# Kernel tuning notes

Measured on AMD Instinct MI355X. Metric: run time of the kernel, lower is better.

## Reference

```python
import jax, jax.numpy as jnp
import numpy as np

BATCH, TIMESTEPS, DIM, OUT = 64, 512, 1024, 1024


def setup_inputs() -> dict:
    key = jax.random.key(0)
    k1, k2, k3, k4, k5, k6 = jax.random.split(key, 6)
    # glorot-normal-ish scales for params
    def glorot(k, shape):
        fan_in, fan_out = shape[0], shape[-1]
        std = (2.0 / (fan_in + fan_out)) ** 0.5
        return jax.random.normal(k, shape, dtype=jnp.float32) * std
    return {
        "inputs": jax.random.normal(k1, (BATCH, TIMESTEPS, DIM), dtype=jnp.float32),
        "prev_state": jax.random.normal(k2, (BATCH, OUT), dtype=jnp.float32),
        "Wa": glorot(k3, (OUT, OUT)),
        "Ua": glorot(k4, (DIM, OUT)),
        "Va": glorot(k5, (OUT, 1)),
        "Ba": glorot(k6, (1, OUT)),
    }


def reference(inputs, prev_state, Wa, Ua, Va, Ba):
    # WaS: [B, 1, OUT] broadcast over timesteps
    WaS = jnp.einsum("bo,op->bp", prev_state, Wa)[:, None, :]
    # UaH: [B, T, OUT]
    UaH = jnp.einsum("btd,do->bto", inputs, Ua)
    scores = jnp.tanh(UaH + WaS + Ba)            # [B, T, OUT]
    scores = jax.nn.relu(scores @ Va)            # [B, T, 1]
    sm = jax.nn.softmax(scores, axis=1)          # softmax over timesteps
    context_vector = jnp.sum(inputs * sm, axis=1)  # [B, DIM]
    return context_vector
```

## Files before the change

### kernel.cpp

```cpp
#include <hip/hip_runtime.h>


#define NBATCH 64
#define NT     512
#define NDIM   1024
#define NOUT   1024

typedef _Float16 h8 __attribute__((ext_vector_type(8)));
typedef _Float16 h4 __attribute__((ext_vector_type(4)));
typedef float f16v __attribute__((ext_vector_type(16)));

__device__ __forceinline__ float tanh_fast(float x) {
    float e = __expf(2.0f * x);
    return 1.0f - 2.0f * __builtin_amdgcn_rcpf(e + 1.0f);
}

__global__ __launch_bounds__(256) void k_pack_ua(const float* __restrict__ Ua,
                                                 _Float16* __restrict__ B16) {
    int t = blockIdx.x * 256 + threadIdx.x;
    int nn = t & 31, kg = (t >> 5) & 1, ks = (t >> 6) & 63, nt = t >> 12;
    int n = (nt << 5) + nn;
    int kbase = (ks << 4) + (kg << 3);
    h8 v;
#pragma unroll
    for (int j = 0; j < 8; ++j) v[j] = (_Float16)Ua[(size_t)(kbase + j) * 1024 + n];
    *(h8*)(B16 + ((size_t)t << 3)) = v;
}

__global__ __launch_bounds__(256) void k_was_part(const float* __restrict__ ps,
                                                  const float* __restrict__ Wa,
                                                  float* __restrict__ part) {
    int oc = blockIdx.x, b = blockIdx.y, tid = threadIdx.x;
    const float4* Wa4 = (const float4*)Wa;
    const float* psb = ps + b * 1024;
    float4 acc = {0.f, 0.f, 0.f, 0.f};
    int o0 = oc * 128;
#pragma unroll 4
    for (int o = o0; o < o0 + 128; ++o) {
        float s = psb[o];
        float4 wv = Wa4[o * 256 + tid];
        acc.x += s * wv.x; acc.y += s * wv.y; acc.z += s * wv.z; acc.w += s * wv.w;
    }
    ((float4*)part)[((oc << 6) + b) * 256 + tid] = acc;
}

__global__ __launch_bounds__(256) void k_was_reduce(const float* __restrict__ part,
                                                    const float* __restrict__ Ba,
                                                    float* __restrict__ wsWaS) {
    int b = blockIdx.x, tid = threadIdx.x;
    const float4* p4 = (const float4*)part;
    float4 acc = ((const float4*)Ba)[tid];
#pragma unroll
    for (int oc = 0; oc < 8; ++oc) {
        float4 v = p4[((oc << 6) + b) * 256 + tid];
        acc.x += v.x; acc.y += v.y; acc.z += v.z; acc.w += v.w;
    }
    ((float4*)wsWaS)[b * 256 + tid] = acc;
}

#define ASH_STRIDE 136
__global__ __launch_bounds__(256, 2) void k_fused_gemm(
    const float* __restrict__ inputs, const _Float16* __restrict__ B16,
    const float* __restrict__ wsWaS, const float* __restrict__ Va,
    float* __restrict__ scores)
{
    __shared__ _Float16 Ash[2][64 * ASH_STRIDE];
    __shared__ float scoreSh[64];
    const int tid = threadIdx.x;
    const int lane = tid & 63, wv = tid >> 6;
    const int l31 = lane & 31, lhi = lane >> 5;
    const int r0 = blockIdx.x * 64;
    const int b = r0 >> 9;
    const int srow = tid >> 2, sq = tid & 3;
    const float4* srcBase = (const float4*)inputs + (size_t)(r0 + srow) * 256 + sq * 8;

    if (tid < 64) scoreSh[tid] = 0.0f;

    float4 vA[8];
#pragma unroll
    for (int j = 0; j < 8; ++j) vA[j] = srcBase[j];
    {
        _Float16* dst = &Ash[0][srow * ASH_STRIDE + sq * 32];
#pragma unroll
        for (int j = 0; j < 8; ++j) {
            float4 v = vA[j];
            *(h4*)(dst + j * 4) =
                (h4){ (_Float16)v.x, (_Float16)v.y, (_Float16)v.z, (_Float16)v.w };
        }
    }
    __syncthreads();

    for (int pass = 0; pass < 2; ++pass) {
        const int c0w = pass * 512 + wv * 128;
        const int ntb = c0w >> 5;
        f16v acc[2][4];
#pragma unroll
        for (int rt = 0; rt < 2; ++rt)
#pragma unroll
            for (int ct = 0; ct < 4; ++ct)
#pragma unroll
                for (int e = 0; e < 16; ++e) acc[rt][ct][e] = 0.0f;

        for (int kc = 0; kc < 8; ++kc) {
            const int buf = kc & 1;
            const bool pf = !(pass == 1 && kc == 7);
            if (pf) {
                const float4* src = srcBase + (((kc + 1) & 7) << 5);
#pragma unroll
                for (int j = 0; j < 8; ++j) vA[j] = src[j];
            }
#pragma unroll
            for (int ks8 = 0; ks8 < 8; ++ks8) {
                const int ks = kc * 8 + ks8;
                h8 a0 = *(const h8*)&Ash[buf][l31 * ASH_STRIDE + ks8 * 16 + lhi * 8];
                h8 a1 = *(const h8*)&Ash[buf][(32 + l31) * ASH_STRIDE + ks8 * 16 + lhi * 8];
                h8 bf[4];
#pragma unroll
                for (int ct = 0; ct < 4; ++ct)
                    bf[ct] = *(const h8*)(B16 +
                        ((size_t)(((ntb + ct) << 6) + ks) << 9) + lane * 8);
#pragma unroll
                for (int ct = 0; ct < 4; ++ct) {
                    acc[0][ct] = __builtin_amdgcn_mfma_f32_32x32x16_f16(a0, bf[ct], acc[0][ct], 0, 0, 0);
                    acc[1][ct] = __builtin_amdgcn_mfma_f32_32x32x16_f16(a1, bf[ct], acc[1][ct], 0, 0, 0);
                }
            }
            if (pf) {
                _Float16* dst = &Ash[buf ^ 1][srow * ASH_STRIDE + sq * 32];
#pragma unroll
                for (int j = 0; j < 8; ++j) {
                    float4 v = vA[j];
                    *(h4*)(dst + j * 4) =
                        (h4){ (_Float16)v.x, (_Float16)v.y, (_Float16)v.z, (_Float16)v.w };
                }
            }
            __syncthreads();
        }
        float wsv[4], vav[4];
#pragma unroll
        for (int ct = 0; ct < 4; ++ct) {
            int n = c0w + ct * 32 + l31;
            wsv[ct] = wsWaS[b * 1024 + n];
            vav[ct] = Va[n];
        }
#pragma unroll
        for (int rt = 0; rt < 2; ++rt) {
#pragma unroll
            for (int i = 0; i < 16; ++i) {
                float s = 0.0f;
#pragma unroll
                for (int ct = 0; ct < 4; ++ct)
                    s += tanh_fast(acc[rt][ct][i] + wsv[ct]) * vav[ct];
                s += __shfl_xor(s, 1);
                s += __shfl_xor(s, 2);
                s += __shfl_xor(s, 4);
                s += __shfl_xor(s, 8);
                s += __shfl_xor(s, 16);
                if (l31 == 0) {
                    int row = rt * 32 + (i & 3) + ((i >> 2) << 3) + (lhi << 2);
                    atomicAdd(&scoreSh[row], s);
                }
            }
        }
    }
    __syncthreads();
    if (tid < 64) scores[r0 + tid] = fmaxf(scoreSh[tid], 0.0f);
}

__global__ __launch_bounds__(256) void k_softmax(const float* __restrict__ scores,
                                                 float* __restrict__ sm) {
    int b = blockIdx.x, tid = threadIdx.x;
    __shared__ float red[256];
    const float* sb = scores + b * 512;
    float s0 = sb[tid], s1 = sb[tid + 256];
    red[tid] = fmaxf(s0, s1);
    __syncthreads();
    for (int st = 128; st > 0; st >>= 1) {
        if (tid < st) red[tid] = fmaxf(red[tid], red[tid + st]);
        __syncthreads();
    }
    float m = red[0];
    __syncthreads();
    float e0 = __expf(s0 - m), e1 = __expf(s1 - m);
    red[tid] = e0 + e1;
    __syncthreads();
    for (int st = 128; st > 0; st >>= 1) {
        if (tid < st) red[tid] += red[tid + st];
        __syncthreads();
    }
    float inv = 1.0f / red[0];
    sm[b * 512 + tid] = e0 * inv;
    sm[b * 512 + 256 + tid] = e1 * inv;
}

__global__ __launch_bounds__(256) void k_ctx_part(const float* __restrict__ inputs,
                                                  const float* __restrict__ sm,
                                                  float* __restrict__ part) {
    int ts = blockIdx.x, b = blockIdx.y, tid = threadIdx.x;
    const float4* inF4 = (const float4*)inputs;
    float4 acc = {0.f, 0.f, 0.f, 0.f};
    int t0 = ts * 64;
#pragma unroll 8
    for (int t = t0; t < t0 + 64; ++t) {
        float wgt = sm[b * 512 + t];
        float4 x = inF4[(size_t)(b * 512 + t) * 256 + tid];
        acc.x += wgt * x.x; acc.y += wgt * x.y; acc.z += wgt * x.z; acc.w += wgt * x.w;
    }
    ((float4*)part)[((ts << 6) + b) * 256 + tid] = acc;
}

__global__ __launch_bounds__(256) void k_ctx_reduce(const float* __restrict__ part,
                                                    float* __restrict__ out) {
    int g = blockIdx.x * 256 + threadIdx.x;
    const float4* p4 = (const float4*)part;
    float4 acc = p4[g];
#pragma unroll
    for (int s = 1; s < 8; ++s) {
        float4 v = p4[s * 16384 + g];
        acc.x += v.x; acc.y += v.y; acc.z += v.z; acc.w += v.w;
    }
    ((float4*)out)[g] = acc;
}

extern "C" void kernel_launch(void* const* d_in, const int* in_sizes, int n_in,
                              void* d_out, int out_size, void* d_ws, size_t ws_size,
                              hipStream_t stream) {
    const float* inputs = (const float*)d_in[0];
    const float* prev   = (const float*)d_in[1];
    const float* Wa     = (const float*)d_in[2];
    const float* Ua     = (const float*)d_in[3];
    const float* Va     = (const float*)d_in[4];
    const float* Ba     = (const float*)d_in[5];
    float* out = (float*)d_out;

    char* ws = (char*)d_ws;
    _Float16* B16   = (_Float16*)(ws);
    float* wasPart  = (float*)(ws + (2u << 20));
    float* wsWaS    = (float*)(ws + (4u << 20));
    float* scores   = (float*)(ws + (4u << 20) + (256u << 10));
    float* sm       = (float*)(ws + (4u << 20) + (384u << 10));
    float* ctxPart  = (float*)(ws + (4u << 20) + (512u << 10));

    hipLaunchKernelGGL(k_pack_ua,    dim3(512),    dim3(256), 0, stream, Ua, B16);
    hipLaunchKernelGGL(k_was_part,   dim3(8, 64),  dim3(256), 0, stream, prev, Wa, wasPart);
    hipLaunchKernelGGL(k_was_reduce, dim3(64),     dim3(256), 0, stream, wasPart, Ba, wsWaS);
    hipLaunchKernelGGL(k_fused_gemm, dim3(512),    dim3(256), 0, stream, inputs, B16, wsWaS, Va, scores);
    hipLaunchKernelGGL(k_softmax,    dim3(64),     dim3(256), 0, stream, scores, sm);
    hipLaunchKernelGGL(k_ctx_part,   dim3(8, 64),  dim3(256), 0, stream, inputs, sm, ctxPart);
    hipLaunchKernelGGL(k_ctx_reduce, dim3(64),     dim3(256), 0, stream, ctxPart, out);
}
```

Before: 342.6 us.

## Enlarge fused GEMM row tile to 128 and restructure WaS GEMV for weight reuse

The fused GEMM now processes 128 rows per block (4x4 MFMA tiles per wave), so each B fragment loaded from global memory feeds twice as many MFMAs. The cost is a larger accumulator register footprint, occupancy dropping to one block per SM, and only 256 blocks on the device. Because the A tile now covers 128 rows, the inputs tile is reloaded and re-converted to fp16 in each of the two column passes. The WaS kernel is rewritten so each block keeps 32 Wa rows in registers and reuses them across 16 batches, accumulating partial sums through global memory, which cuts redundant Wa reads but launches only 32 blocks.

```diff
diff --git a/kernel.cpp b/kernel.cpp
--- a/kernel.cpp
+++ b/kernel.cpp
@@ -1,10 +1,5 @@
 #include <hip/hip_runtime.h>
 
-
-#define NBATCH 64
-#define NT     512
-#define NDIM   1024
-#define NOUT   1024
 
 typedef _Float16 h8 __attribute__((ext_vector_type(8)));
 typedef _Float16 h4 __attribute__((ext_vector_type(4)));
@@ -30,18 +25,34 @@
 __global__ __launch_bounds__(256) void k_was_part(const float* __restrict__ ps,
                                                   const float* __restrict__ Wa,
                                                   float* __restrict__ part) {
-    int oc = blockIdx.x, b = blockIdx.y, tid = threadIdx.x;
+    int ic = blockIdx.x >> 2, psl = blockIdx.x & 3;
+    int tid = threadIdx.x, wv = tid >> 6, lane = tid & 63;
+    int p4 = psl * 64 + lane;
     const float4* Wa4 = (const float4*)Wa;
-    const float* psb = ps + b * 1024;
-    float4 acc = {0.f, 0.f, 0.f, 0.f};
-    int o0 = oc * 128;
-#pragma unroll 4
-    for (int o = o0; o < o0 + 128; ++o) {
-        float s = psb[o];
-        float4 wv = Wa4[o * 256 + tid];
-        acc.x += s * wv.x; acc.y += s * wv.y; acc.z += s * wv.z; acc.w += s * wv.w;
-    }
-    ((float4*)part)[((oc << 6) + b) * 256 + tid] = acc;
+    float4* part4 = (float4*)part;
+#pragma unroll 1
+    for (int c = 0; c < 4; ++c) {
+        int o0 = ic * 128 + c * 32;
+        float4 w[32];
+#pragma unroll
+        for (int o = 0; o < 32; ++o) w[o] = Wa4[(size_t)(o0 + o) * 256 + p4];
+#pragma unroll 1
+        for (int bb = 0; bb < 16; ++bb) {
+            int b = wv * 16 + bb;
+            const float* psb = ps + b * 1024 + o0;
+            size_t oidx = (size_t)((ic << 6) + b) * 256 + p4;
+            float4 a;
+            if (c == 0) { a.x = a.y = a.z = a.w = 0.f; }
+            else        { a = part4[oidx]; }
+#pragma unroll
+            for (int o = 0; o < 32; ++o) {
+                float s = psb[o];
+                a.x += s * w[o].x; a.y += s * w[o].y;
+                a.z += s * w[o].z; a.w += s * w[o].w;
+            }
+            part4[oidx] = a;
+        }
+    }
 }
 
 __global__ __launch_bounds__(256) void k_was_reduce(const float* __restrict__ part,
@@ -51,100 +62,103 @@
     const float4* p4 = (const float4*)part;
     float4 acc = ((const float4*)Ba)[tid];
 #pragma unroll
-    for (int oc = 0; oc < 8; ++oc) {
-        float4 v = p4[((oc << 6) + b) * 256 + tid];
+    for (int ic = 0; ic < 8; ++ic) {
+        float4 v = p4[((ic << 6) + b) * 256 + tid];
         acc.x += v.x; acc.y += v.y; acc.z += v.z; acc.w += v.w;
     }
     ((float4*)wsWaS)[b * 256 + tid] = acc;
 }
 
-#define ASH_STRIDE 136
-__global__ __launch_bounds__(256, 2) void k_fused_gemm(
+#define AST 136
+__global__ __launch_bounds__(256, 1) void k_fused_gemm(
     const float* __restrict__ inputs, const _Float16* __restrict__ B16,
     const float* __restrict__ wsWaS, const float* __restrict__ Va,
     float* __restrict__ scores)
 {
-    __shared__ _Float16 Ash[2][64 * ASH_STRIDE];
-    __shared__ float scoreSh[64];
+    __shared__ _Float16 Ash[2][128 * AST];
+    __shared__ float scoreSh[128];
     const int tid = threadIdx.x;
     const int lane = tid & 63, wv = tid >> 6;
     const int l31 = lane & 31, lhi = lane >> 5;
-    const int r0 = blockIdx.x * 64;
+    const int r0 = blockIdx.x * 128;
     const int b = r0 >> 9;
-    const int srow = tid >> 2, sq = tid & 3;
-    const float4* srcBase = (const float4*)inputs + (size_t)(r0 + srow) * 256 + sq * 8;
-
-    if (tid < 64) scoreSh[tid] = 0.0f;
-
-    float4 vA[8];
-#pragma unroll
-    for (int j = 0; j < 8; ++j) vA[j] = srcBase[j];
-    {
-        _Float16* dst = &Ash[0][srow * ASH_STRIDE + sq * 32];
-#pragma unroll
-        for (int j = 0; j < 8; ++j) {
-            float4 v = vA[j];
-            *(h4*)(dst + j * 4) =
-                (h4){ (_Float16)v.x, (_Float16)v.y, (_Float16)v.z, (_Float16)v.w };
-        }
-    }
-    __syncthreads();
+    const int srow = tid >> 1, sq = tid & 1;
+    const float4* srcBase = (const float4*)inputs + (size_t)(r0 + srow) * 256 + sq * 16;
+
+    if (tid < 128) scoreSh[tid] = 0.0f;
 
     for (int pass = 0; pass < 2; ++pass) {
-        const int c0w = pass * 512 + wv * 128;
-        const int ntb = c0w >> 5;
-        f16v acc[2][4];
-#pragma unroll
-        for (int rt = 0; rt < 2; ++rt)
+        const int ntb = (pass << 4) + (wv << 2);
+        f16v acc[4][4];
+#pragma unroll
+        for (int rt = 0; rt < 4; ++rt)
 #pragma unroll
             for (int ct = 0; ct < 4; ++ct)
 #pragma unroll
                 for (int e = 0; e < 16; ++e) acc[rt][ct][e] = 0.0f;
+
+        float4 vA[16];
+#pragma unroll
+        for (int j = 0; j < 16; ++j) vA[j] = srcBase[j];
+        {
+            _Float16* dst = &Ash[0][srow * AST + sq * 64];
+#pragma unroll
+            for (int j = 0; j < 8; ++j) {
+                float4 v0 = vA[2 * j], v1 = vA[2 * j + 1];
+                *(h8*)(dst + j * 8) = (h8){ (_Float16)v0.x, (_Float16)v0.y,
+                                            (_Float16)v0.z, (_Float16)v0.w,
+                                            (_Float16)v1.x, (_Float16)v1.y,
+                                            (_Float16)v1.z, (_Float16)v1.w };
+            }
+        }
+        __syncthreads();
 
         for (int kc = 0; kc < 8; ++kc) {
             const int buf = kc & 1;
-            const bool pf = !(pass == 1 && kc == 7);
-            if (pf) {
-                const float4* src = srcBase + (((kc + 1) & 7) << 5);
-#pragma unroll
-                for (int j = 0; j < 8; ++j) vA[j] = src[j];
+            if (kc < 7) {
+                const float4* s2 = srcBase + ((kc + 1) << 5);
+#pragma unroll
+                for (int j = 0; j < 16; ++j) vA[j] = s2[j];
             }
 #pragma unroll
             for (int ks8 = 0; ks8 < 8; ++ks8) {
-                const int ks = kc * 8 + ks8;
-                h8 a0 = *(const h8*)&Ash[buf][l31 * ASH_STRIDE + ks8 * 16 + lhi * 8];
-                h8 a1 = *(const h8*)&Ash[buf][(32 + l31) * ASH_STRIDE + ks8 * 16 + lhi * 8];
-                h8 bf[4];
+                const int ks = (kc << 3) + ks8;
+                h8 af[4], bf[4];
+#pragma unroll
+                for (int rt = 0; rt < 4; ++rt)
+                    af[rt] = *(const h8*)&Ash[buf][(rt * 32 + l31) * AST + ks8 * 16 + lhi * 8];
 #pragma unroll
                 for (int ct = 0; ct < 4; ++ct)
-                    bf[ct] = *(const h8*)(B16 +
-                        ((size_t)(((ntb + ct) << 6) + ks) << 9) + lane * 8);
-#pragma unroll
-                for (int ct = 0; ct < 4; ++ct) {
-                    acc[0][ct] = __builtin_amdgcn_mfma_f32_32x32x16_f16(a0, bf[ct], acc[0][ct], 0, 0, 0);
-                    acc[1][ct] = __builtin_amdgcn_mfma_f32_32x32x16_f16(a1, bf[ct], acc[1][ct], 0, 0, 0);
+                    bf[ct] = *(const h8*)(B16 + ((((ntb + ct) << 6) + ks) << 9) + lane * 8);
+#pragma unroll
+                for (int rt = 0; rt < 4; ++rt)
+#pragma unroll
+                    for (int ct = 0; ct < 4; ++ct)
+                        acc[rt][ct] = __builtin_amdgcn_mfma_f32_32x32x16_f16(
+                            af[rt], bf[ct], acc[rt][ct], 0, 0, 0);
+            }
+            if (kc < 7) {
+                _Float16* dst = &Ash[buf ^ 1][srow * AST + sq * 64];
+#pragma unroll
+                for (int j = 0; j < 8; ++j) {
+                    float4 v0 = vA[2 * j], v1 = vA[2 * j + 1];
+                    *(h8*)(dst + j * 8) = (h8){ (_Float16)v0.x, (_Float16)v0.y,
+                                                (_Float16)v0.z, (_Float16)v0.w,
+                                                (_Float16)v1.x, (_Float16)v1.y,
+                                                (_Float16)v1.z, (_Float16)v1.w };
                 }
             }
-            if (pf) {
-                _Float16* dst = &Ash[buf ^ 1][srow * ASH_STRIDE + sq * 32];
-#pragma unroll
-                for (int j = 0; j < 8; ++j) {
-                    float4 v = vA[j];
-                    *(h4*)(dst + j * 4) =
-                        (h4){ (_Float16)v.x, (_Float16)v.y, (_Float16)v.z, (_Float16)v.w };
-                }
-            }
             __syncthreads();
         }
         float wsv[4], vav[4];
 #pragma unroll
         for (int ct = 0; ct < 4; ++ct) {
-            int n = c0w + ct * 32 + l31;
+            int n = (pass << 9) + (wv << 7) + (ct << 5) + l31;
             wsv[ct] = wsWaS[b * 1024 + n];
             vav[ct] = Va[n];
         }
 #pragma unroll
-        for (int rt = 0; rt < 2; ++rt) {
+        for (int rt = 0; rt < 4; ++rt) {
 #pragma unroll
             for (int i = 0; i < 16; ++i) {
                 float s = 0.0f;
@@ -164,7 +178,7 @@
         }
     }
     __syncthreads();
-    if (tid < 64) scores[r0 + tid] = fmaxf(scoreSh[tid], 0.0f);
+    if (tid < 128) scores[r0 + tid] = fmaxf(scoreSh[tid], 0.0f);
 }
 
 __global__ __launch_bounds__(256) void k_softmax(const float* __restrict__ scores,
@@ -242,9 +256,9 @@
     float* ctxPart  = (float*)(ws + (4u << 20) + (512u << 10));
 
     hipLaunchKernelGGL(k_pack_ua,    dim3(512),    dim3(256), 0, stream, Ua, B16);
-    hipLaunchKernelGGL(k_was_part,   dim3(8, 64),  dim3(256), 0, stream, prev, Wa, wasPart);
+    hipLaunchKernelGGL(k_was_part,   dim3(32),     dim3(256), 0, stream, prev, Wa, wasPart);
     hipLaunchKernelGGL(k_was_reduce, dim3(64),     dim3(256), 0, stream, wasPart, Ba, wsWaS);
-    hipLaunchKernelGGL(k_fused_gemm, dim3(512),    dim3(256), 0, stream, inputs, B16, wsWaS, Va, scores);
+    hipLaunchKernelGGL(k_fused_gemm, dim3(256),    dim3(256), 0, stream, inputs, B16, wsWaS, Va, scores);
     hipLaunchKernelGGL(k_softmax,    dim3(64),     dim3(256), 0, stream, scores, sm);
     hipLaunchKernelGGL(k_ctx_part,   dim3(8, 64),  dim3(256), 0, stream, inputs, sm, ctxPart);
     hipLaunchKernelGGL(k_ctx_reduce, dim3(64),     dim3(256), 0, stream, ctxPart, out);
```

New measurement: 388.3 us. +13.3%, slower.
